# Kernel tuning notes

Measured on AMD Instinct MI355X. Metric: run time of the kernel, lower is better.

The kernel has to match this reference:

```python
import jax, jax.numpy as jnp
import numpy as np

B, N, D_IN = 256, 64, 128   # batch, n_agents, input_dim
H0, H1, H2 = 256, 256, 64   # rnn_hidden_dim[0], [1], [2]


def setup_inputs() -> dict:
    key = jax.random.key(0)
    ks = jax.random.split(key, 14)
    s = 0.05
    return {
        "obs": jax.random.normal(ks[0], (B, N, D_IN), dtype=jnp.float32),
        "W_enc": jax.random.normal(ks[1], (H0, D_IN), dtype=jnp.float32) * s,
        "b_enc": jax.random.normal(ks[2], (H0,), dtype=jnp.float32) * s,
        "W_obs": jax.random.normal(ks[3], (H0, H0), dtype=jnp.float32) * s,
        "b_obs": jax.random.normal(ks[4], (H0,), dtype=jnp.float32) * s,
        "W_ih": jax.random.normal(ks[5], (3 * H0, H0), dtype=jnp.float32) * s,
        "b_ih": jax.random.normal(ks[6], (3 * H0,), dtype=jnp.float32) * s,
        "W_hh": jax.random.normal(ks[7], (3 * H0, H0), dtype=jnp.float32) * s,
        "b_hh": jax.random.normal(ks[8], (3 * H0,), dtype=jnp.float32) * s,
        "W_val": jax.random.normal(ks[9], (H1, H0), dtype=jnp.float32) * s,
        "b_val": jax.random.normal(ks[10], (H1,), dtype=jnp.float32) * s,
        "W_dec": jax.random.normal(ks[11], (H2, H1), dtype=jnp.float32) * s,
        "b_dec": jax.random.normal(ks[12], (H2,), dtype=jnp.float32) * s,
    }


def reference(obs, W_enc, b_enc, W_obs, b_obs, W_ih, b_ih, W_hh, b_hh,
              W_val, b_val, W_dec, b_dec):
    # encoding + f_obs  -> h: [B, N, H0]
    x = jax.nn.relu(jnp.einsum("bnd,hd->bnh", obs, W_enc) + b_enc)
    h = jnp.einsum("bnh,gh->bng", x, W_obs) + b_obs

    # comm: mean over other agents. Original masks self and divides by N
    # (mean over dim of size N with self zeroed) => (sum_all - self) / N.
    c = (jnp.sum(h, axis=1, keepdims=True) - h) / N  # [B, N, H0]

    # GRUCell(input=c, hidden=h), PyTorch gate ordering r, z, n
    gi = jnp.einsum("bnh,gh->bng", c, W_ih) + b_ih   # [B, N, 3*H0]
    gh = jnp.einsum("bnh,gh->bng", h, W_hh) + b_hh
    gi_r, gi_z, gi_n = jnp.split(gi, 3, axis=-1)
    gh_r, gh_z, gh_n = jnp.split(gh, 3, axis=-1)
    r = jax.nn.sigmoid(gi_r + gh_r)
    z = jax.nn.sigmoid(gi_z + gh_z)
    n = jnp.tanh(gi_n + r * gh_n)
    h = (1.0 - z) * n + z * h  # [B, N, H0]

    # value head + decoding; seq_len=1 squeezed -> [B, N, H2]
    v = jnp.einsum("bnh,vh->bnv", h, W_val) + b_val
    out = jnp.einsum("bnv,ov->bno", v, W_dec) + b_dec
    return out
```

## Files before the change

### kernel.cpp

```cpp
#include <hip/hip_runtime.h>
#include <hip/hip_bf16.h>
#include <math.h>


typedef __bf16  bf16x8 __attribute__((ext_vector_type(8)));
typedef float   f32x4  __attribute__((ext_vector_type(4)));

#define DIN 128
#define H0  256

#define O_WENC 0
#define O_WOBS 32768
#define O_WIH  98304
#define O_WHH  294912
#define O_WVAL 491520
#define O_WDEC 557056
#define W_TOT  573440

__device__ __forceinline__ f32x4 mfma16(bf16x8 a, bf16x8 b, f32x4 c) {
    return __builtin_amdgcn_mfma_f32_16x16x32_bf16(a, b, c, 0, 0, 0);
}
__device__ __forceinline__ float bf2f(__hip_bfloat16 x) { return __bfloat162float(x); }
__device__ __forceinline__ __hip_bfloat16 f2bf(float x) { return __float2bfloat16(x); }
__device__ __forceinline__ float sigmoidf_(float x) { return 1.0f / (1.0f + expf(-x)); }

__device__ __forceinline__ bf16x8 w8(const __hip_bfloat16* p, int idx) {
    return *(const bf16x8*)(p + idx);
}

__device__ __forceinline__ int tadr(int r, int k) {
    return (r << 8) + ((((k >> 3) ^ r) & 31) << 3) + (k & 7);
}
__device__ __forceinline__ int oadr(int r, int k) {
    return (r << 7) + ((((k >> 3) ^ r) & 15) << 3) + (k & 7);
}

__global__ __launch_bounds__(256) void prep_kernel(
    const float* __restrict__ W_enc, const float* __restrict__ W_obs,
    const float* __restrict__ W_ih,  const float* __restrict__ W_hh,
    const float* __restrict__ W_val, const float* __restrict__ W_dec,
    __hip_bfloat16* __restrict__ ws)
{
    const int i = (blockIdx.x * 256 + threadIdx.x) * 8;
    if (i >= W_TOT) return;
    const float* src; int off;
    if      (i < O_WOBS) { src = W_enc; off = O_WENC; }
    else if (i < O_WIH)  { src = W_obs; off = O_WOBS; }
    else if (i < O_WHH)  { src = W_ih;  off = O_WIH;  }
    else if (i < O_WVAL) { src = W_hh;  off = O_WHH;  }
    else if (i < O_WDEC) { src = W_val; off = O_WVAL; }
    else                 { src = W_dec; off = O_WDEC; }
    const float* f = src + (i - off);
    f32x4 a = *(const f32x4*)f;
    f32x4 b = *(const f32x4*)(f + 4);
    bf16x8 v;
    #pragma unroll
    for (int j = 0; j < 4; j++) { v[j] = (__bf16)a[j]; v[j + 4] = (__bf16)b[j]; }
    *(bf16x8*)(ws + i) = v;
}

__global__ __launch_bounds__(512, 2) void commnet_mfma(
    const __hip_bfloat16* __restrict__ ws,
    const float* __restrict__ b_enc, const float* __restrict__ b_obs,
    const float* __restrict__ b_ih,  const float* __restrict__ b_hh,
    const float* __restrict__ b_val, const float* __restrict__ b_dec,
    const float* __restrict__ obs,   float* __restrict__ out)
{
    __shared__ __align__(16) __hip_bfloat16 T0[64 * 256];
    __shared__ __align__(16) __hip_bfloat16 T1[64 * 256];

    const __hip_bfloat16* W_enc = ws + O_WENC;
    const __hip_bfloat16* W_obs = ws + O_WOBS;
    const __hip_bfloat16* W_ih  = ws + O_WIH;
    const __hip_bfloat16* W_hh  = ws + O_WHH;
    const __hip_bfloat16* W_val = ws + O_WVAL;
    const __hip_bfloat16* W_dec = ws + O_WDEC;

    const int tid  = threadIdx.x;
    const int wave = tid >> 6;
    const int lane = tid & 63;
    const int quad = lane >> 4;
    const int lc   = lane & 15;
    const int row0 = blockIdx.x * 64;
    const int ko16 = quad * 8;

    for (int i = tid; i < 64 * DIN / 8; i += 512) {
        const int r = i >> 4;
        const int c = (i & 15) << 3;
        const float* src = obs + (row0 + r) * DIN + c;
        f32x4 a = *(const f32x4*)src;
        f32x4 b = *(const f32x4*)(src + 4);
        bf16x8 v;
        #pragma unroll
        for (int j = 0; j < 4; j++) { v[j] = (__bf16)a[j]; v[j + 4] = (__bf16)b[j]; }
        *(bf16x8*)&T1[oadr(r, c)] = v;
    }
    __syncthreads();

    #pragma unroll
    for (int cp = 0; cp < 2; cp++) {
        const int n = (wave + 8 * cp) * 16 + lc;
        const float bias = b_enc[n];
        f32x4 acc[4] = {};
        #pragma unroll
        for (int k0 = 0; k0 < DIN; k0 += 32) {
            const int kk = k0 + ko16;
            bf16x8 b = w8(W_enc, n * DIN + kk);
            #pragma unroll
            for (int rt = 0; rt < 4; rt++) {
                bf16x8 a = *(const bf16x8*)&T1[oadr(rt * 16 + lc, kk)];
                acc[rt] = mfma16(a, b, acc[rt]);
            }
        }
        #pragma unroll
        for (int rt = 0; rt < 4; rt++)
            #pragma unroll
            for (int i = 0; i < 4; i++) {
                const int row = rt * 16 + quad * 4 + i;
                T0[tadr(row, n)] = f2bf(fmaxf(acc[rt][i] + bias, 0.0f));
            }
    }
    __syncthreads();

    #pragma unroll
    for (int cp = 0; cp < 2; cp++) {
        const int n = (wave + 8 * cp) * 16 + lc;
        const float bias = b_obs[n];
        f32x4 acc[4] = {};
        #pragma unroll 2
        for (int k0 = 0; k0 < H0; k0 += 32) {
            const int kk = k0 + ko16;
            bf16x8 b = w8(W_obs, n * H0 + kk);
            #pragma unroll
            for (int rt = 0; rt < 4; rt++) {
                bf16x8 a = *(const bf16x8*)&T0[tadr(rt * 16 + lc, kk)];
                acc[rt] = mfma16(a, b, acc[rt]);
            }
        }
        #pragma unroll
        for (int rt = 0; rt < 4; rt++)
            #pragma unroll
            for (int i = 0; i < 4; i++) {
                const int row = rt * 16 + quad * 4 + i;
                T1[tadr(row, n)] = f2bf(acc[rt][i] + bias);
            }
    }
    __syncthreads();

    #pragma unroll
    for (int cp = 0; cp < 2; cp++) {
        const int n = (wave + 8 * cp) * 16 + lc;
        const float bir = b_ih[n], biz = b_ih[n + 256], bin = b_ih[n + 512];
        const float bhr = b_hh[n], bhz = b_hh[n + 256], bhn = b_hh[n + 512];
        f32x4 gir[4] = {}, giz[4] = {}, gin[4] = {};
        f32x4 ghr[4] = {}, ghz[4] = {}, ghn[4] = {};
        #pragma unroll 2
        for (int k0 = 0; k0 < H0; k0 += 32) {
            const int kk = k0 + ko16;
            bf16x8 bir8 = w8(W_ih, (n      ) * H0 + kk);
            bf16x8 biz8 = w8(W_ih, (n + 256) * H0 + kk);
            bf16x8 bin8 = w8(W_ih, (n + 512) * H0 + kk);
            bf16x8 bhr8 = w8(W_hh, (n      ) * H0 + kk);
            bf16x8 bhz8 = w8(W_hh, (n + 256) * H0 + kk);
            bf16x8 bhn8 = w8(W_hh, (n + 512) * H0 + kk);
            #pragma unroll
            for (int rt = 0; rt < 4; rt++) {
                bf16x8 aH = *(const bf16x8*)&T1[tadr(rt * 16 + lc, kk)];
                gir[rt] = mfma16(aH, bir8, gir[rt]);
                giz[rt] = mfma16(aH, biz8, giz[rt]);
                gin[rt] = mfma16(aH, bin8, gin[rt]);
                ghr[rt] = mfma16(aH, bhr8, ghr[rt]);
                ghz[rt] = mfma16(aH, bhz8, ghz[rt]);
                ghn[rt] = mfma16(aH, bhn8, ghn[rt]);
            }
        }
        float Sr = 0.0f, Sz = 0.0f, Sn = 0.0f;
        #pragma unroll
        for (int rt = 0; rt < 4; rt++)
            #pragma unroll
            for (int i = 0; i < 4; i++) {
                Sr += gir[rt][i]; Sz += giz[rt][i]; Sn += gin[rt][i];
            }
        Sr += __shfl_xor(Sr, 16); Sr += __shfl_xor(Sr, 32);
        Sz += __shfl_xor(Sz, 16); Sz += __shfl_xor(Sz, 32);
        Sn += __shfl_xor(Sn, 16); Sn += __shfl_xor(Sn, 32);

        #pragma unroll
        for (int rt = 0; rt < 4; rt++)
            #pragma unroll
            for (int i = 0; i < 4; i++) {
                const int row = rt * 16 + quad * 4 + i;
                const float gi_r = (Sr - gir[rt][i]) * (1.0f / 64.0f) + bir;
                const float gi_z = (Sz - giz[rt][i]) * (1.0f / 64.0f) + biz;
                const float gi_n = (Sn - gin[rt][i]) * (1.0f / 64.0f) + bin;
                const float r  = sigmoidf_(gi_r + ghr[rt][i] + bhr);
                const float z  = sigmoidf_(gi_z + ghz[rt][i] + bhz);
                const float nn = tanhf(gi_n + r * (ghn[rt][i] + bhn));
                const float h  = bf2f(T1[tadr(row, n)]);
                T0[tadr(row, n)] = f2bf((1.0f - z) * nn + z * h);
            }
    }
    __syncthreads();

    #pragma unroll
    for (int cp = 0; cp < 2; cp++) {
        const int n = (wave + 8 * cp) * 16 + lc;
        const float bias = b_val[n];
        f32x4 acc[4] = {};
        #pragma unroll 2
        for (int k0 = 0; k0 < H0; k0 += 32) {
            const int kk = k0 + ko16;
            bf16x8 b = w8(W_val, n * H0 + kk);
            #pragma unroll
            for (int rt = 0; rt < 4; rt++) {
                bf16x8 a = *(const bf16x8*)&T0[tadr(rt * 16 + lc, kk)];
                acc[rt] = mfma16(a, b, acc[rt]);
            }
        }
        #pragma unroll
        for (int rt = 0; rt < 4; rt++)
            #pragma unroll
            for (int i = 0; i < 4; i++) {
                const int row = rt * 16 + quad * 4 + i;
                T1[tadr(row, n)] = f2bf(acc[rt][i] + bias);
            }
    }
    __syncthreads();

    {
        const int ct  = wave & 3;
        const int rtb = (wave >> 2) * 2;
        const int n   = ct * 16 + lc;
        const float bias = b_dec[n];
        f32x4 acc[2] = {};
        #pragma unroll 2
        for (int k0 = 0; k0 < H0; k0 += 32) {
            const int kk = k0 + ko16;
            bf16x8 b = w8(W_dec, n * H0 + kk);
            #pragma unroll
            for (int j = 0; j < 2; j++) {
                bf16x8 a = *(const bf16x8*)&T1[tadr((rtb + j) * 16 + lc, kk)];
                acc[j] = mfma16(a, b, acc[j]);
            }
        }
        #pragma unroll
        for (int j = 0; j < 2; j++)
            #pragma unroll
            for (int i = 0; i < 4; i++) {
                const int row = (rtb + j) * 16 + quad * 4 + i;
                out[(row0 + row) * 64 + n] = acc[j][i] + bias;
            }
    }
}

extern "C" void kernel_launch(void* const* d_in, const int* in_sizes, int n_in,
                              void* d_out, int out_size, void* d_ws, size_t ws_size,
                              hipStream_t stream) {
    (void)in_sizes; (void)n_in; (void)out_size; (void)ws_size;
    const float* obs   = (const float*)d_in[0];
    const float* W_enc = (const float*)d_in[1];  const float* b_enc = (const float*)d_in[2];
    const float* W_obs = (const float*)d_in[3];  const float* b_obs = (const float*)d_in[4];
    const float* W_ih  = (const float*)d_in[5];  const float* b_ih  = (const float*)d_in[6];
    const float* W_hh  = (const float*)d_in[7];  const float* b_hh  = (const float*)d_in[8];
    const float* W_val = (const float*)d_in[9];  const float* b_val = (const float*)d_in[10];
    const float* W_dec = (const float*)d_in[11]; const float* b_dec = (const float*)d_in[12];
    float* out = (float*)d_out;
    __hip_bfloat16* ws = (__hip_bfloat16*)d_ws;

    prep_kernel<<<280, 256, 0, stream>>>(W_enc, W_obs, W_ih, W_hh, W_val, W_dec, ws);
    commnet_mfma<<<256, 512, 0, stream>>>(
        ws, b_enc, b_obs, b_ih, b_hh, b_val, b_dec, obs, out);
}
```

Baseline: 128.4 us.

## Fuse weight bf16 conversion into main kernel, use 1024-thread blocks and fast gates

Removes the separate weight-conversion prep kernel and converts fp32 weights to bf16 inside the main kernel as they are loaded. Each block now runs 16 waves, one column tile per wave, and the GRU gate GEMMs are split into an r/z phase and an n phase to cut register pressure. Sigmoid and tanh use hardware exp2/rcp intrinsics. This trades the second launch and workspace traffic for twice the weight bytes read per block, plus lower occupancy per CU and slightly less accurate activations.

```diff
diff --git a/kernel.cpp b/kernel.cpp
--- a/kernel.cpp
+++ b/kernel.cpp
@@ -8,24 +8,30 @@
 
 #define DIN 128
 #define H0  256
-
-#define O_WENC 0
-#define O_WOBS 32768
-#define O_WIH  98304
-#define O_WHH  294912
-#define O_WVAL 491520
-#define O_WDEC 557056
-#define W_TOT  573440
+#define LOG2E 1.44269504088896f
 
 __device__ __forceinline__ f32x4 mfma16(bf16x8 a, bf16x8 b, f32x4 c) {
     return __builtin_amdgcn_mfma_f32_16x16x32_bf16(a, b, c, 0, 0, 0);
 }
 __device__ __forceinline__ float bf2f(__hip_bfloat16 x) { return __bfloat162float(x); }
 __device__ __forceinline__ __hip_bfloat16 f2bf(float x) { return __float2bfloat16(x); }
-__device__ __forceinline__ float sigmoidf_(float x) { return 1.0f / (1.0f + expf(-x)); }
-
-__device__ __forceinline__ bf16x8 w8(const __hip_bfloat16* p, int idx) {
-    return *(const bf16x8*)(p + idx);
+
+__device__ __forceinline__ float fsigmoid(float x) {
+    float e = __builtin_amdgcn_exp2f(-LOG2E * x);
+    return __builtin_amdgcn_rcpf(1.0f + e);
+}
+__device__ __forceinline__ float ftanh(float x) {
+    float e = __builtin_amdgcn_exp2f(2.0f * LOG2E * x);
+    return 1.0f - 2.0f * __builtin_amdgcn_rcpf(1.0f + e);
+}
+
+__device__ __forceinline__ bf16x8 w8f(const float* __restrict__ p, int idx) {
+    f32x4 a = *(const f32x4*)(p + idx);
+    f32x4 b = *(const f32x4*)(p + idx + 4);
+    bf16x8 r;
+    #pragma unroll
+    for (int j = 0; j < 4; j++) { r[j] = (__bf16)a[j]; r[j + 4] = (__bf16)b[j]; }
+    return r;
 }
 
 __device__ __forceinline__ int tadr(int r, int k) {
@@ -35,46 +41,18 @@
     return (r << 7) + ((((k >> 3) ^ r) & 15) << 3) + (k & 7);
 }
 
-__global__ __launch_bounds__(256) void prep_kernel(
-    const float* __restrict__ W_enc, const float* __restrict__ W_obs,
-    const float* __restrict__ W_ih,  const float* __restrict__ W_hh,
-    const float* __restrict__ W_val, const float* __restrict__ W_dec,
-    __hip_bfloat16* __restrict__ ws)
-{
-    const int i = (blockIdx.x * 256 + threadIdx.x) * 8;
-    if (i >= W_TOT) return;
-    const float* src; int off;
-    if      (i < O_WOBS) { src = W_enc; off = O_WENC; }
-    else if (i < O_WIH)  { src = W_obs; off = O_WOBS; }
-    else if (i < O_WHH)  { src = W_ih;  off = O_WIH;  }
-    else if (i < O_WVAL) { src = W_hh;  off = O_WHH;  }
-    else if (i < O_WDEC) { src = W_val; off = O_WVAL; }
-    else                 { src = W_dec; off = O_WDEC; }
-    const float* f = src + (i - off);
-    f32x4 a = *(const f32x4*)f;
-    f32x4 b = *(const f32x4*)(f + 4);
-    bf16x8 v;
-    #pragma unroll
-    for (int j = 0; j < 4; j++) { v[j] = (__bf16)a[j]; v[j + 4] = (__bf16)b[j]; }
-    *(bf16x8*)(ws + i) = v;
-}
-
-__global__ __launch_bounds__(512, 2) void commnet_mfma(
-    const __hip_bfloat16* __restrict__ ws,
-    const float* __restrict__ b_enc, const float* __restrict__ b_obs,
-    const float* __restrict__ b_ih,  const float* __restrict__ b_hh,
-    const float* __restrict__ b_val, const float* __restrict__ b_dec,
-    const float* __restrict__ obs,   float* __restrict__ out)
+__global__ __launch_bounds__(1024, 1) void commnet_mfma(
+    const float* __restrict__ obs,
+    const float* __restrict__ W_enc, const float* __restrict__ b_enc,
+    const float* __restrict__ W_obs, const float* __restrict__ b_obs,
+    const float* __restrict__ W_ih,  const float* __restrict__ b_ih,
+    const float* __restrict__ W_hh,  const float* __restrict__ b_hh,
+    const float* __restrict__ W_val, const float* __restrict__ b_val,
+    const float* __restrict__ W_dec, const float* __restrict__ b_dec,
+    float* __restrict__ out)
 {
     __shared__ __align__(16) __hip_bfloat16 T0[64 * 256];
     __shared__ __align__(16) __hip_bfloat16 T1[64 * 256];
-
-    const __hip_bfloat16* W_enc = ws + O_WENC;
-    const __hip_bfloat16* W_obs = ws + O_WOBS;
-    const __hip_bfloat16* W_ih  = ws + O_WIH;
-    const __hip_bfloat16* W_hh  = ws + O_WHH;
-    const __hip_bfloat16* W_val = ws + O_WVAL;
-    const __hip_bfloat16* W_dec = ws + O_WDEC;
 
     const int tid  = threadIdx.x;
     const int wave = tid >> 6;
@@ -83,10 +61,11 @@
     const int lc   = lane & 15;
     const int row0 = blockIdx.x * 64;
     const int ko16 = quad * 8;
-
-    for (int i = tid; i < 64 * DIN / 8; i += 512) {
-        const int r = i >> 4;
-        const int c = (i & 15) << 3;
+    const int n    = wave * 16 + lc;
+
+    {
+        const int r = tid >> 4;
+        const int c = (tid & 15) << 3;
         const float* src = obs + (row0 + r) * DIN + c;
         f32x4 a = *(const f32x4*)src;
         f32x4 b = *(const f32x4*)(src + 4);
@@ -97,15 +76,13 @@
     }
     __syncthreads();
 
-    #pragma unroll
-    for (int cp = 0; cp < 2; cp++) {
-        const int n = (wave + 8 * cp) * 16 + lc;
+    {
         const float bias = b_enc[n];
         f32x4 acc[4] = {};
         #pragma unroll
         for (int k0 = 0; k0 < DIN; k0 += 32) {
             const int kk = k0 + ko16;
-            bf16x8 b = w8(W_enc, n * DIN + kk);
+            bf16x8 b = w8f(W_enc, n * DIN + kk);
             #pragma unroll
             for (int rt = 0; rt < 4; rt++) {
                 bf16x8 a = *(const bf16x8*)&T1[oadr(rt * 16 + lc, kk)];
@@ -122,15 +99,13 @@
     }
     __syncthreads();
 
-    #pragma unroll
-    for (int cp = 0; cp < 2; cp++) {
-        const int n = (wave + 8 * cp) * 16 + lc;
+    {
         const float bias = b_obs[n];
         f32x4 acc[4] = {};
         #pragma unroll 2
         for (int k0 = 0; k0 < H0; k0 += 32) {
             const int kk = k0 + ko16;
-            bf16x8 b = w8(W_obs, n * H0 + kk);
+            bf16x8 b = w8f(W_obs, n * H0 + kk);
             #pragma unroll
             for (int rt = 0; rt < 4; rt++) {
                 bf16x8 a = *(const bf16x8*)&T0[tadr(rt * 16 + lc, kk)];
@@ -147,44 +122,34 @@
     }
     __syncthreads();
 
-    #pragma unroll
-    for (int cp = 0; cp < 2; cp++) {
-        const int n = (wave + 8 * cp) * 16 + lc;
-        const float bir = b_ih[n], biz = b_ih[n + 256], bin = b_ih[n + 512];
-        const float bhr = b_hh[n], bhz = b_hh[n + 256], bhn = b_hh[n + 512];
-        f32x4 gir[4] = {}, giz[4] = {}, gin[4] = {};
-        f32x4 ghr[4] = {}, ghz[4] = {}, ghn[4] = {};
-        #pragma unroll 2
-        for (int k0 = 0; k0 < H0; k0 += 32) {
-            const int kk = k0 + ko16;
-            bf16x8 bir8 = w8(W_ih, (n      ) * H0 + kk);
-            bf16x8 biz8 = w8(W_ih, (n + 256) * H0 + kk);
-            bf16x8 bin8 = w8(W_ih, (n + 512) * H0 + kk);
-            bf16x8 bhr8 = w8(W_hh, (n      ) * H0 + kk);
-            bf16x8 bhz8 = w8(W_hh, (n + 256) * H0 + kk);
-            bf16x8 bhn8 = w8(W_hh, (n + 512) * H0 + kk);
+    f32x4 zreg[4];
+    {
+        const float bir = b_ih[n], biz = b_ih[n + 256];
+        const float bhr = b_hh[n], bhz = b_hh[n + 256];
+        f32x4 gir[4] = {}, giz[4] = {}, ghr[4] = {}, ghz[4] = {};
+        #pragma unroll 2
+        for (int k0 = 0; k0 < H0; k0 += 32) {
+            const int kk = k0 + ko16;
+            bf16x8 bir8 = w8f(W_ih, (n      ) * H0 + kk);
+            bf16x8 biz8 = w8f(W_ih, (n + 256) * H0 + kk);
+            bf16x8 bhr8 = w8f(W_hh, (n      ) * H0 + kk);
+            bf16x8 bhz8 = w8f(W_hh, (n + 256) * H0 + kk);
             #pragma unroll
             for (int rt = 0; rt < 4; rt++) {
                 bf16x8 aH = *(const bf16x8*)&T1[tadr(rt * 16 + lc, kk)];
                 gir[rt] = mfma16(aH, bir8, gir[rt]);
                 giz[rt] = mfma16(aH, biz8, giz[rt]);
-                gin[rt] = mfma16(aH, bin8, gin[rt]);
                 ghr[rt] = mfma16(aH, bhr8, ghr[rt]);
                 ghz[rt] = mfma16(aH, bhz8, ghz[rt]);
-                ghn[rt] = mfma16(aH, bhn8, ghn[rt]);
-            }
-        }
-        float Sr = 0.0f, Sz = 0.0f, Sn = 0.0f;
-        #pragma unroll
-        for (int rt = 0; rt < 4; rt++)
-            #pragma unroll
-            for (int i = 0; i < 4; i++) {
-                Sr += gir[rt][i]; Sz += giz[rt][i]; Sn += gin[rt][i];
-            }
+            }
+        }
+        float Sr = 0.0f, Sz = 0.0f;
+        #pragma unroll
+        for (int rt = 0; rt < 4; rt++)
+            #pragma unroll
+            for (int i = 0; i < 4; i++) { Sr += gir[rt][i]; Sz += giz[rt][i]; }
         Sr += __shfl_xor(Sr, 16); Sr += __shfl_xor(Sr, 32);
         Sz += __shfl_xor(Sz, 16); Sz += __shfl_xor(Sz, 32);
-        Sn += __shfl_xor(Sn, 16); Sn += __shfl_xor(Sn, 32);
-
         #pragma unroll
         for (int rt = 0; rt < 4; rt++)
             #pragma unroll
@@ -192,25 +157,53 @@
                 const int row = rt * 16 + quad * 4 + i;
                 const float gi_r = (Sr - gir[rt][i]) * (1.0f / 64.0f) + bir;
                 const float gi_z = (Sz - giz[rt][i]) * (1.0f / 64.0f) + biz;
+                T0[tadr(row, n)] = f2bf(fsigmoid(gi_r + ghr[rt][i] + bhr));
+                zreg[rt][i]      = fsigmoid(gi_z + ghz[rt][i] + bhz);
+            }
+    }
+    {
+        const float bin = b_ih[n + 512], bhn = b_hh[n + 512];
+        f32x4 gin[4] = {}, ghn[4] = {};
+        #pragma unroll 2
+        for (int k0 = 0; k0 < H0; k0 += 32) {
+            const int kk = k0 + ko16;
+            bf16x8 bin8 = w8f(W_ih, (n + 512) * H0 + kk);
+            bf16x8 bhn8 = w8f(W_hh, (n + 512) * H0 + kk);
+            #pragma unroll
+            for (int rt = 0; rt < 4; rt++) {
+                bf16x8 aH = *(const bf16x8*)&T1[tadr(rt * 16 + lc, kk)];
+                gin[rt] = mfma16(aH, bin8, gin[rt]);
+                ghn[rt] = mfma16(aH, bhn8, ghn[rt]);
+            }
+        }
+        float Sn = 0.0f;
+        #pragma unroll
+        for (int rt = 0; rt < 4; rt++)
+            #pragma unroll
+            for (int i = 0; i < 4; i++) Sn += gin[rt][i];
+        Sn += __shfl_xor(Sn, 16); Sn += __shfl_xor(Sn, 32);
+        #pragma unroll
+        for (int rt = 0; rt < 4; rt++)
+            #pragma unroll
+            for (int i = 0; i < 4; i++) {
+                const int row = rt * 16 + quad * 4 + i;
                 const float gi_n = (Sn - gin[rt][i]) * (1.0f / 64.0f) + bin;
-                const float r  = sigmoidf_(gi_r + ghr[rt][i] + bhr);
-                const float z  = sigmoidf_(gi_z + ghz[rt][i] + bhz);
-                const float nn = tanhf(gi_n + r * (ghn[rt][i] + bhn));
+                const float rr = bf2f(T0[tadr(row, n)]);
+                const float nn = ftanh(gi_n + rr * (ghn[rt][i] + bhn));
+                const float z  = zreg[rt][i];
                 const float h  = bf2f(T1[tadr(row, n)]);
                 T0[tadr(row, n)] = f2bf((1.0f - z) * nn + z * h);
             }
     }
     __syncthreads();
 
-    #pragma unroll
-    for (int cp = 0; cp < 2; cp++) {
-        const int n = (wave + 8 * cp) * 16 + lc;
+    {
         const float bias = b_val[n];
         f32x4 acc[4] = {};
         #pragma unroll 2
         for (int k0 = 0; k0 < H0; k0 += 32) {
             const int kk = k0 + ko16;
-            bf16x8 b = w8(W_val, n * H0 + kk);
+            bf16x8 b = w8f(W_val, n * H0 + kk);
             #pragma unroll
             for (int rt = 0; rt < 4; rt++) {
                 bf16x8 a = *(const bf16x8*)&T0[tadr(rt * 16 + lc, kk)];
@@ -228,46 +221,37 @@
     __syncthreads();
 
     {
-        const int ct  = wave & 3;
-        const int rtb = (wave >> 2) * 2;
-        const int n   = ct * 16 + lc;
-        const float bias = b_dec[n];
-        f32x4 acc[2] = {};
-        #pragma unroll 2
-        for (int k0 = 0; k0 < H0; k0 += 32) {
-            const int kk = k0 + ko16;
-            bf16x8 b = w8(W_dec, n * H0 + kk);
-            #pragma unroll
-            for (int j = 0; j < 2; j++) {
-                bf16x8 a = *(const bf16x8*)&T1[tadr((rtb + j) * 16 + lc, kk)];
-                acc[j] = mfma16(a, b, acc[j]);
-            }
-        }
-        #pragma unroll
-        for (int j = 0; j < 2; j++)
-            #pragma unroll
-            for (int i = 0; i < 4; i++) {
-                const int row = (rtb + j) * 16 + quad * 4 + i;
-                out[(row0 + row) * 64 + n] = acc[j][i] + bias;
-            }
+        const int ct = wave & 3;
+        const int rg = wave >> 2;
+        const int nd = ct * 16 + lc;
+        const float bias = b_dec[nd];
+        f32x4 acc = {};
+        #pragma unroll 2
+        for (int k0 = 0; k0 < H0; k0 += 32) {
+            const int kk = k0 + ko16;
+            bf16x8 b = w8f(W_dec, nd * H0 + kk);
+            bf16x8 a = *(const bf16x8*)&T1[tadr(rg * 16 + lc, kk)];
+            acc = mfma16(a, b, acc);
+        }
+        #pragma unroll
+        for (int i = 0; i < 4; i++) {
+            const int row = rg * 16 + quad * 4 + i;
+            out[(row0 + row) * 64 + nd] = acc[i] + bias;
+        }
     }
 }
 
 extern "C" void kernel_launch(void* const* d_in, const int* in_sizes, int n_in,
                               void* d_out, int out_size, void* d_ws, size_t ws_size,
                               hipStream_t stream) {
-    (void)in_sizes; (void)n_in; (void)out_size; (void)ws_size;
-    const float* obs   = (const float*)d_in[0];
-    const float* W_enc = (const float*)d_in[1];  const float* b_enc = (const float*)d_in[2];
-    const float* W_obs = (const float*)d_in[3];  const float* b_obs = (const float*)d_in[4];
-    const float* W_ih  = (const float*)d_in[5];  const float* b_ih  = (const float*)d_in[6];
-    const float* W_hh  = (const float*)d_in[7];  const float* b_hh  = (const float*)d_in[8];
-    const float* W_val = (const float*)d_in[9];  const float* b_val = (const float*)d_in[10];
-    const float* W_dec = (const float*)d_in[11]; const float* b_dec = (const float*)d_in[12];
-    float* out = (float*)d_out;
-    __hip_bfloat16* ws = (__hip_bfloat16*)d_ws;
-
-    prep_kernel<<<280, 256, 0, stream>>>(W_enc, W_obs, W_ih, W_hh, W_val, W_dec, ws);
-    commnet_mfma<<<256, 512, 0, stream>>>(
-        ws, b_enc, b_obs, b_ih, b_hh, b_val, b_dec, obs, out);
-}
+    (void)in_sizes; (void)n_in; (void)out_size; (void)d_ws; (void)ws_size;
+    commnet_mfma<<<256, 1024, 0, stream>>>(
+        (const float*)d_in[0],
+        (const float*)d_in[1],  (const float*)d_in[2],
+        (const float*)d_in[3],  (const float*)d_in[4],
+        (const float*)d_in[5],  (const float*)d_in[6],
+        (const float*)d_in[7],  (const float*)d_in[8],
+        (const float*)d_in[9],  (const float*)d_in[10],
+        (const float*)d_in[11], (const float*)d_in[12],
+        (float*)d_out);
+}
```

Measured after the change: 171.8 us. +33.8%, slower.
